# Kernel optimization log

Measured on AMD Instinct MI355X. Metric: run time of the kernel, lower is better.

## Reference

```python
import jax, jax.numpy as jnp
import numpy as np

NUM_HEADS = 16
HEAD_DIM = 64
D_DEC = 1024
D_ENC = 1024
R = 256  # kv_lora_rank
LN_EPS = 1e-5


def setup_inputs() -> dict:
    key = jax.random.key(0)
    ks = jax.random.split(key, 8)
    B, SQ, SK = 4, 2048, 4096
    query = jax.random.normal(ks[0], (B, SQ, D_DEC), dtype=jnp.float32)
    encoder_output = jax.random.normal(ks[1], (B, SK, D_ENC), dtype=jnp.float32)
    s = 0.02
    Wq = jax.random.normal(ks[2], (NUM_HEADS * HEAD_DIM, D_DEC), dtype=jnp.float32) * s
    Wkva = jax.random.normal(ks[3], (R, D_ENC), dtype=jnp.float32) * s
    ln_g = jnp.ones((R,), dtype=jnp.float32)
    ln_b = jnp.zeros((R,), dtype=jnp.float32)
    Wkvb = jax.random.normal(ks[4], (NUM_HEADS * 2 * HEAD_DIM, R), dtype=jnp.float32) * s
    Wout = jax.random.normal(ks[5], (D_DEC, NUM_HEADS * HEAD_DIM), dtype=jnp.float32) * s
    return {"query": query, "encoder_output": encoder_output, "Wq": Wq,
            "Wkva": Wkva, "ln_g": ln_g, "ln_b": ln_b, "Wkvb": Wkvb, "Wout": Wout}


def reference(query, encoder_output, Wq, Wkva, ln_g, ln_b, Wkvb, Wout):
    B, SQ, _ = query.shape
    SK = encoder_output.shape[1]
    H, Dh = NUM_HEADS, HEAD_DIM

    # q projection -> [B, H, SQ, Dh]
    q = jnp.einsum('bsd,ed->bse', query, Wq).reshape(B, SQ, H, Dh).transpose(0, 2, 1, 3)

    # low-rank KV compression + layernorm
    c = jnp.einsum('bsd,rd->bsr', encoder_output, Wkva)  # [B, SK, R]
    mu = jnp.mean(c, axis=-1, keepdims=True)
    var = jnp.mean(jnp.square(c - mu), axis=-1, keepdims=True)
    c = (c - mu) * jax.lax.rsqrt(var + LN_EPS) * ln_g + ln_b

    # decompress to K,V: [B, SK, H, 2*Dh] -> split
    kv = jnp.einsum('bsr,er->bse', c, Wkvb).reshape(B, SK, H, 2 * Dh).transpose(0, 2, 1, 3)
    k, v = kv[..., :Dh], kv[..., Dh:]

    scale = 1.0 / np.sqrt(Dh).astype(np.float32)
    scores = jnp.einsum('bhqd,bhkd->bhqk', q, k) * scale
    attn = jax.nn.softmax(scores, axis=-1)  # dropout is identity in eval / p=0
    o = jnp.einsum('bhqk,bhkd->bhqd', attn, v)
    o = o.transpose(0, 2, 1, 3).reshape(B, SQ, H * Dh)
    return jnp.einsum('bse,de->bsd', o, Wout)
```

## Files before the change

kernel.cpp:

```cpp
#include <hip/hip_runtime.h>

#define LOG2E 1.4426950408889634f

typedef __attribute__((ext_vector_type(8))) short short8;
typedef __attribute__((ext_vector_type(4))) float f32x4;

__device__ inline unsigned short f2bf(float f) {
  unsigned u = __float_as_uint(f);
  u += 0x7fffu + ((u >> 16) & 1u);
  return (unsigned short)(u >> 16);
}

#define MFMA16(a, b, c) __builtin_amdgcn_mfma_f32_16x16x32_bf16((a), (b), (c), 0, 0, 0)

#define GLDS16(gp, lp)                                                              \
  __builtin_amdgcn_global_load_lds((const __attribute__((address_space(1))) void*)(gp), \
                                   (__attribute__((address_space(3))) void*)(lp), 16, 0, 0)

__device__ inline f32x4 zero4() {
  f32x4 z = {0.f, 0.f, 0.f, 0.f};
  return z;
}

__global__ __launch_bounds__(256) void k_cast6(
    const float* __restrict__ e, const float* __restrict__ q, const float* __restrict__ wq,
    const float* __restrict__ wo, const float* __restrict__ wb, const float* __restrict__ wa,
    unsigned short* __restrict__ eo, unsigned short* __restrict__ qo, unsigned short* __restrict__ wqo,
    unsigned short* __restrict__ woo, unsigned short* __restrict__ wbo, unsigned short* __restrict__ wao) {
  int i = (blockIdx.x * 256 + threadIdx.x) * 4;
  const float* src;
  unsigned short* dst;
  int off;
  if (i < 16777216) { src = e; dst = eo; off = i; }
  else if (i < 25165824) { src = q; dst = qo; off = i - 16777216; }
  else if (i < 26214400) { src = wq; dst = wqo; off = i - 25165824; }
  else if (i < 27262976) { src = wo; dst = woo; off = i - 26214400; }
  else if (i < 27787264) { src = wb; dst = wbo; off = i - 27262976; }
  else { src = wa; dst = wao; off = i - 27787264; }
  float4 v = *(const float4*)(src + off);
  unsigned lo = (unsigned)f2bf(v.x) | ((unsigned)f2bf(v.y) << 16);
  unsigned hi = (unsigned)f2bf(v.z) | ((unsigned)f2bf(v.w) << 16);
  *(uint2*)(dst + off) = make_uint2(lo, hi);
}

__global__ __launch_bounds__(256, 2) void k_qproj(const unsigned short* __restrict__ A,
                                                  const unsigned short* __restrict__ Bw,
                                                  unsigned short* __restrict__ Qout) {
  __shared__ __align__(16) short As[128 * 32];
  __shared__ __align__(16) short Bs[128 * 32];
  const int K = 1024;
  int tid = threadIdx.x;
  int w = tid >> 6, lane = tid & 63, quad = lane >> 4, c = lane & 15;
  int m0 = blockIdx.x * 128, n0 = blockIdx.y * 128;
  int wm = (w >> 1) * 64, wn = (w & 1) * 64;
  f32x4 acc[4][4];
#pragma unroll
  for (int i = 0; i < 4; i++)
#pragma unroll
    for (int j = 0; j < 4; j++) acc[i][j] = zero4();

  for (int k0 = 0; k0 < K; k0 += 32) {
#pragma unroll
    for (int i = 0; i < 2; i++) {
      int seg = w * 2 + i;
      int bo = seg * 1024 + lane * 16;
      int row = bo >> 6, col = (bo & 63) >> 1;
      GLDS16(A + (size_t)(m0 + row) * K + k0 + col, (char*)As + seg * 1024);
      GLDS16(Bw + (size_t)(n0 + row) * K + k0 + col, (char*)Bs + seg * 1024);
    }
    __syncthreads();
    short8 af[4], bfr[4];
#pragma unroll
    for (int i = 0; i < 4; i++) {
      af[i] = *(const short8*)&As[(wm + i * 16 + c) * 32 + quad * 8];
      bfr[i] = *(const short8*)&Bs[(wn + i * 16 + c) * 32 + quad * 8];
    }
#pragma unroll
    for (int mi = 0; mi < 4; mi++)
#pragma unroll
      for (int ni = 0; ni < 4; ni++) acc[mi][ni] = MFMA16(af[mi], bfr[ni], acc[mi][ni]);
    __syncthreads();
  }
  const float scale = 0.125f * LOG2E;
#pragma unroll
  for (int mi = 0; mi < 4; mi++) {
    int rowb = m0 + wm + mi * 16 + quad * 4;
#pragma unroll
    for (int ni = 0; ni < 4; ni++) {
      int col = n0 + wn + ni * 16 + c;
      int h = col >> 6, d = col & 63;
#pragma unroll
      for (int r = 0; r < 4; r++) {
        int row = rowb + r;
        int b = row >> 11, sq = row & 2047;
        Qout[(((size_t)(b * 16 + h)) * 2048 + sq) * 64 + d] = f2bf(acc[mi][ni][r] * scale);
      }
    }
  }
}

__global__ __launch_bounds__(256, 2) void k_cln(const unsigned short* __restrict__ E,
                                                const unsigned short* __restrict__ Wa,
                                                const float* __restrict__ g, const float* __restrict__ bb,
                                                unsigned short* __restrict__ Cout) {
  __shared__ __align__(16) short As[64 * 32];
  __shared__ __align__(16) short Bs[256 * 32];
  __shared__ float redS[4][64], redQ[4][64];
  __shared__ float gS[256], bS[256];
  const int K = 1024;
  int tid = threadIdx.x;
  int w = tid >> 6, lane = tid & 63, quad = lane >> 4, c = lane & 15;
  int m0 = blockIdx.x * 64;
  gS[tid] = g[tid];
  bS[tid] = bb[tid];
  f32x4 acc[4][4];
#pragma unroll
  for (int i = 0; i < 4; i++)
#pragma unroll
    for (int j = 0; j < 4; j++) acc[i][j] = zero4();

  for (int k0 = 0; k0 < K; k0 += 32) {
    {
      int bo = w * 1024 + lane * 16;
      int row = bo >> 6, col = (bo & 63) >> 1;
      GLDS16(E + (size_t)(m0 + row) * K + k0 + col, (char*)As + w * 1024);
    }
#pragma unroll
    for (int i = 0; i < 4; i++) {
      int seg = w * 4 + i;
      int bo = seg * 1024 + lane * 16;
      int row = bo >> 6, col = (bo & 63) >> 1;
      GLDS16(Wa + (size_t)row * K + k0 + col, (char*)Bs + seg * 1024);
    }
    __syncthreads();
    short8 af[4], bfr[4];
#pragma unroll
    for (int i = 0; i < 4; i++) {
      af[i] = *(const short8*)&As[(i * 16 + c) * 32 + quad * 8];
      bfr[i] = *(const short8*)&Bs[(w * 64 + i * 16 + c) * 32 + quad * 8];
    }
#pragma unroll
    for (int mi = 0; mi < 4; mi++)
#pragma unroll
      for (int ni = 0; ni < 4; ni++) acc[mi][ni] = MFMA16(af[mi], bfr[ni], acc[mi][ni]);
    __syncthreads();
  }
  float ps[4][4], pq[4][4];
#pragma unroll
  for (int mi = 0; mi < 4; mi++)
#pragma unroll
    for (int r = 0; r < 4; r++) {
      float s = 0.f, q = 0.f;
#pragma unroll
      for (int ni = 0; ni < 4; ni++) {
        float x = acc[mi][ni][r];
        s += x;
        q += x * x;
      }
      for (int m = 1; m < 16; m <<= 1) {
        s += __shfl_xor(s, m, 64);
        q += __shfl_xor(q, m, 64);
      }
      ps[mi][r] = s;
      pq[mi][r] = q;
    }
  if (c == 0) {
#pragma unroll
    for (int mi = 0; mi < 4; mi++)
#pragma unroll
      for (int r = 0; r < 4; r++) {
        int row = mi * 16 + quad * 4 + r;
        redS[w][row] = ps[mi][r];
        redQ[w][row] = pq[mi][r];
      }
  }
  __syncthreads();
  float muv[4][4], rsv[4][4];
#pragma unroll
  for (int mi = 0; mi < 4; mi++)
#pragma unroll
    for (int r = 0; r < 4; r++) {
      int row = mi * 16 + quad * 4 + r;
      float S = redS[0][row] + redS[1][row] + redS[2][row] + redS[3][row];
      float Q = redQ[0][row] + redQ[1][row] + redQ[2][row] + redQ[3][row];
      float mu = S * (1.f / 256.f);
      float var = Q * (1.f / 256.f) - mu * mu;
      muv[mi][r] = mu;
      rsv[mi][r] = rsqrtf(var + 1e-5f);
    }
#pragma unroll
  for (int mi = 0; mi < 4; mi++)
#pragma unroll
    for (int ni = 0; ni < 4; ni++) {
      int col = w * 64 + ni * 16 + c;
#pragma unroll
      for (int r = 0; r < 4; r++) {
        int row = m0 + mi * 16 + quad * 4 + r;
        float y = (acc[mi][ni][r] - muv[mi][r]) * rsv[mi][r] * gS[col] + bS[col];
        Cout[(size_t)row * 256 + col] = f2bf(y);
      }
    }
}

__global__ __launch_bounds__(256, 2) void k_kv(const unsigned short* __restrict__ A,
                                               const unsigned short* __restrict__ Bw,
                                               unsigned short* __restrict__ Kb,
                                               unsigned short* __restrict__ Vb) {
  __shared__ __align__(16) short As[128 * 32];
  __shared__ __align__(16) short Bs[128 * 32];
  const int K = 256;
  int tid = threadIdx.x;
  int w = tid >> 6, lane = tid & 63, quad = lane >> 4, c = lane & 15;
  int m0 = blockIdx.x * 128, n0 = blockIdx.y * 128;
  int wm = (w >> 1) * 64, wn = (w & 1) * 64;
  f32x4 acc[4][4];
#pragma unroll
  for (int i = 0; i < 4; i++)
#pragma unroll
    for (int j = 0; j < 4; j++) acc[i][j] = zero4();

  for (int k0 = 0; k0 < K; k0 += 32) {
#pragma unroll
    for (int i = 0; i < 2; i++) {
      int seg = w * 2 + i;
      int bo = seg * 1024 + lane * 16;
      int row = bo >> 6, col = (bo & 63) >> 1;
      GLDS16(A + (size_t)(m0 + row) * K + k0 + col, (char*)As + seg * 1024);
      GLDS16(Bw + (size_t)(n0 + row) * K + k0 + col, (char*)Bs + seg * 1024);
    }
    __syncthreads();
    short8 af[4], bfr[4];
#pragma unroll
    for (int i = 0; i < 4; i++) {
      af[i] = *(const short8*)&As[(wm + i * 16 + c) * 32 + quad * 8];
      bfr[i] = *(const short8*)&Bs[(wn + i * 16 + c) * 32 + quad * 8];
    }
#pragma unroll
    for (int mi = 0; mi < 4; mi++)
#pragma unroll
      for (int ni = 0; ni < 4; ni++) acc[mi][ni] = MFMA16(af[mi], bfr[ni], acc[mi][ni]);
    __syncthreads();
  }
#pragma unroll
  for (int mi = 0; mi < 4; mi++) {
    int rowb = m0 + wm + mi * 16 + quad * 4;
#pragma unroll
    for (int ni = 0; ni < 4; ni++) {
      int col = n0 + wn + ni * 16 + c;
      int h = col >> 7, rr = col & 127;
#pragma unroll
      for (int r = 0; r < 4; r++) {
        int row = rowb + r;
        int b = row >> 12, sk = row & 4095;
        float x = acc[mi][ni][r];
        if (rr < 64)
          Kb[(((size_t)(b * 16 + h)) * 4096 + sk) * 64 + rr] = f2bf(x);
        else
          Vb[(((size_t)(b * 16 + h)) * 64 + (rr - 64)) * 4096 + sk] = f2bf(x);
      }
    }
  }
}

__global__ __launch_bounds__(256, 4) void k_attn(const unsigned short* __restrict__ Qb,
                                                 const unsigned short* __restrict__ Kb,
                                                 const unsigned short* __restrict__ Vb,
                                                 unsigned short* __restrict__ Ob) {
  __shared__ __align__(16) short KVs[2 * 64 * 64];
  __shared__ __align__(16) short Ps[4][2048];
  int tid = threadIdx.x;
  int w = tid >> 6, lane = tid & 63, quad = lane >> 4, c = lane & 15;
  int r8 = lane >> 3, pc = lane & 7;
  int qt = blockIdx.x, bh = blockIdx.y;

  const char* Kg = (const char*)Kb + (size_t)bh * 524288;
  const char* Vg = (const char*)Vb + (size_t)bh * 524288;
  const unsigned short* Qv = Qb + ((size_t)bh * 2048 + qt * 128 + w * 32) * 64 + c * 64 + quad * 8;

  const char* sg[4];
  int step = (w < 2) ? 8192 : 128;
#pragma unroll
  for (int i = 0; i < 4; i++) {
    int seg = w * 4 + i;
    if (w < 2) {
      int row = seg * 8 + r8;
      sg[i] = Kg + row * 128 + ((pc ^ r8) << 4);
    } else {
      int vrow = (seg - 8) * 8 + r8;
      sg[i] = Vg + (size_t)vrow * 8192 + ((pc ^ r8) << 4);
    }
  }

  int c7 = c & 7;
  int kb0 = c * 128 + ((quad ^ c7) << 4);
  int kb1 = c * 128 + (((quad + 4) ^ c7) << 4);
  const char* KsB0 = (const char*)KVs + kb0;
  const char* KsB1 = (const char*)KVs + kb1;
  const char* VsB0 = (const char*)KVs + 8192 + kb0;
  const char* VsB1 = (const char*)KVs + 8192 + kb1;
  char* pwm[4];
#pragma unroll
  for (int mt = 0; mt < 4; mt++)
    pwm[mt] = (char*)Ps[w] + c * 128 + (quad & 1) * 8 + ((((mt * 2) ^ (quad >> 1) ^ c7)) << 4);
  const char* pr0 = (const char*)Ps[w] + c * 128 + ((quad ^ c7) << 4);
  const char* pr1 = (const char*)Ps[w] + c * 128 + (((quad + 4) ^ c7) << 4);

  short8 qf[2][2];
#pragma unroll
  for (int nt = 0; nt < 2; nt++)
#pragma unroll
    for (int h = 0; h < 2; h++) qf[nt][h] = *(const short8*)(Qv + nt * 1024 + h * 32);

  f32x4 O[2][4];
  float lp[2] = {0.f, 0.f};
#pragma unroll
  for (int i = 0; i < 2; i++)
#pragma unroll
    for (int j = 0; j < 4; j++) O[i][j] = zero4();

#pragma unroll
  for (int i = 0; i < 4; i++) {
    GLDS16(sg[i], (char*)KVs + (w * 4 + i) * 1024);
    sg[i] += step;
  }

  for (int kt = 0; kt < 64; kt++) {
    __syncthreads();
#pragma unroll
    for (int mt = 0; mt < 4; mt++) {
      short8 kf0 = *(const short8*)(KsB0 + mt * 2048);
      short8 kf1 = *(const short8*)(KsB1 + mt * 2048);
      f32x4 s0 = MFMA16(kf0, qf[0][0], zero4());
      s0 = MFMA16(kf1, qf[0][1], s0);
      f32x4 s1 = MFMA16(kf0, qf[1][0], zero4());
      s1 = MFMA16(kf1, qf[1][1], s1);
#pragma unroll
      for (int nt = 0; nt < 2; nt++) {
        f32x4 s = nt ? s1 : s0;
        float p0 = __builtin_amdgcn_exp2f(s[0]);
        float p1 = __builtin_amdgcn_exp2f(s[1]);
        float p2 = __builtin_amdgcn_exp2f(s[2]);
        float p3 = __builtin_amdgcn_exp2f(s[3]);
        lp[nt] += (p0 + p1) + (p2 + p3);
        unsigned r0 = __float_as_uint(p0) + 0x8000u;
        unsigned r1 = __float_as_uint(p1) + 0x8000u;
        unsigned r2 = __float_as_uint(p2) + 0x8000u;
        unsigned r3 = __float_as_uint(p3) + 0x8000u;
        unsigned lo = __builtin_amdgcn_perm(r1, r0, 0x07060302u);
        unsigned hi = __builtin_amdgcn_perm(r3, r2, 0x07060302u);
        *(uint2*)(pwm[mt] + nt * 2048) = make_uint2(lo, hi);
      }
    }
#pragma unroll
    for (int kk = 0; kk < 2; kk++) {
      const char* VsB = kk ? VsB1 : VsB0;
      const char* pr = kk ? pr1 : pr0;
      short8 vf[4];
#pragma unroll
      for (int dt = 0; dt < 4; dt++) vf[dt] = *(const short8*)(VsB + dt * 2048);
#pragma unroll
      for (int mo = 0; mo < 2; mo++) {
        short8 pf = *(const short8*)(pr + mo * 2048);
#pragma unroll
        for (int dt = 0; dt < 4; dt++) O[mo][dt] = MFMA16(pf, vf[dt], O[mo][dt]);
      }
    }
    __syncthreads();
    if (kt < 63) {
#pragma unroll
      for (int i = 0; i < 4; i++) {
        GLDS16(sg[i], (char*)KVs + (w * 4 + i) * 1024);
        sg[i] += step;
      }
    }
  }

#pragma unroll
  for (int nt = 0; nt < 2; nt++) {
    lp[nt] += __shfl_xor(lp[nt], 16, 64);
    lp[nt] += __shfl_xor(lp[nt], 32, 64);
  }
  int b = bh >> 4, h = bh & 15;
#pragma unroll
  for (int mo = 0; mo < 2; mo++) {
#pragma unroll
    for (int r = 0; r < 4; r++) {
      float inv = __builtin_amdgcn_rcpf(__shfl(lp[mo], quad * 4 + r, 64));
      int sq = qt * 128 + w * 32 + mo * 16 + quad * 4 + r;
#pragma unroll
      for (int dt = 0; dt < 4; dt++)
        Ob[((size_t)b * 2048 + sq) * 1024 + h * 64 + dt * 16 + c] = f2bf(O[mo][dt][r] * inv);
    }
  }
}

__global__ __launch_bounds__(256, 2) void k_out(const unsigned short* __restrict__ A,
                                                const unsigned short* __restrict__ Bw,
                                                float* __restrict__ Out) {
  __shared__ __align__(16) short As[128 * 32];
  __shared__ __align__(16) short Bs[128 * 32];
  const int K = 1024;
  int tid = threadIdx.x;
  int w = tid >> 6, lane = tid & 63, quad = lane >> 4, c = lane & 15;
  int m0 = blockIdx.x * 128, n0 = blockIdx.y * 128;
  int wm = (w >> 1) * 64, wn = (w & 1) * 64;
  f32x4 acc[4][4];
#pragma unroll
  for (int i = 0; i < 4; i++)
#pragma unroll
    for (int j = 0; j < 4; j++) acc[i][j] = zero4();

  for (int k0 = 0; k0 < K; k0 += 32) {
#pragma unroll
    for (int i = 0; i < 2; i++) {
      int seg = w * 2 + i;
      int bo = seg * 1024 + lane * 16;
      int row = bo >> 6, col = (bo & 63) >> 1;
      GLDS16(A + (size_t)(m0 + row) * K + k0 + col, (char*)As + seg * 1024);
      GLDS16(Bw + (size_t)(n0 + row) * K + k0 + col, (char*)Bs + seg * 1024);
    }
    __syncthreads();
    short8 af[4], bfr[4];
#pragma unroll
    for (int i = 0; i < 4; i++) {
      af[i] = *(const short8*)&As[(wm + i * 16 + c) * 32 + quad * 8];
      bfr[i] = *(const short8*)&Bs[(wn + i * 16 + c) * 32 + quad * 8];
    }
#pragma unroll
    for (int mi = 0; mi < 4; mi++)
#pragma unroll
      for (int ni = 0; ni < 4; ni++) acc[mi][ni] = MFMA16(af[mi], bfr[ni], acc[mi][ni]);
    __syncthreads();
  }
#pragma unroll
  for (int mi = 0; mi < 4; mi++) {
    int rowb = m0 + wm + mi * 16 + quad * 4;
#pragma unroll
    for (int ni = 0; ni < 4; ni++) {
      int col = n0 + wn + ni * 16 + c;
#pragma unroll
      for (int r = 0; r < 4; r++) Out[(size_t)(rowb + r) * 1024 + col] = acc[mi][ni][r];
    }
  }
}

extern "C" void kernel_launch(void* const* d_in, const int* in_sizes, int n_in,
                              void* d_out, int out_size, void* d_ws, size_t ws_size,
                              hipStream_t stream) {
  const float* query = (const float*)d_in[0];
  const float* enc = (const float*)d_in[1];
  const float* Wq = (const float*)d_in[2];
  const float* Wkva = (const float*)d_in[3];
  const float* ln_g = (const float*)d_in[4];
  const float* ln_b = (const float*)d_in[5];
  const float* Wkvb = (const float*)d_in[6];
  const float* Wout = (const float*)d_in[7];
  if (ws_size < 81264640) return;

  char* ws = (char*)d_ws;
  unsigned short* wq_bf = (unsigned short*)(ws + 0);
  unsigned short* wa_bf = (unsigned short*)(ws + 2097152);
  unsigned short* wb_bf = (unsigned short*)(ws + 2621440);
  unsigned short* wo_bf = (unsigned short*)(ws + 3670016);
  unsigned short* qproj = (unsigned short*)(ws + 5767168);
  unsigned short* cln = (unsigned short*)(ws + 22544384);
  unsigned short* ebf_v = (unsigned short*)(ws + 30932992);
  unsigned short* qin_o = (unsigned short*)(ws + 64487424);
  unsigned short* kbuf = (unsigned short*)d_out;

  k_cast6<<<27392, 256, 0, stream>>>(enc, query, Wq, Wout, Wkvb, Wkva,
                                     ebf_v, qin_o, wq_bf, wo_bf, wb_bf, wa_bf);

  k_qproj<<<dim3(64, 8), 256, 0, stream>>>(qin_o, wq_bf, qproj);
  k_cln<<<256, 256, 0, stream>>>(ebf_v, wa_bf, ln_g, ln_b, cln);
  k_kv<<<dim3(128, 16), 256, 0, stream>>>(cln, wb_bf, kbuf, ebf_v);
  k_attn<<<dim3(16, 64), 256, 0, stream>>>(qproj, kbuf, ebf_v, qin_o);
  k_out<<<dim3(64, 8), 256, 0, stream>>>(qin_o, wo_bf, (float*)d_out);
}
```

Measured before the change: 448.1 us.

## Rewrite attention kernel with 32x32 MFMA, register-resident P and fragment-ordered K/V

The attention kernel moves from 16x16x32 to 32x32x16 bf16 MFMA with 128-thread blocks. Each wave now owns 64 query rows. P is converted with v_cvt_pk_bf16 and rearranged between lanes with permlane32_swap, so it stays in registers instead of passing through an LDS scratch buffer. k_kv now writes K and V already laid out in MFMA fragment order per 64-key tile, which lets them be streamed into a double-buffered LDS with plain linear loads and waited on with explicit vmcnt barriers. This removes LDS round trips and swizzle arithmetic, at the cost of higher register pressure and fewer waves per block.

```diff
diff --git a/kernel.cpp b/kernel.cpp
--- a/kernel.cpp
+++ b/kernel.cpp
@@ -4,6 +4,8 @@
 
 typedef __attribute__((ext_vector_type(8))) short short8;
 typedef __attribute__((ext_vector_type(4))) float f32x4;
+typedef __attribute__((ext_vector_type(16))) float f32x16;
+typedef __attribute__((ext_vector_type(4))) unsigned u32x4;
 
 __device__ inline unsigned short f2bf(float f) {
   unsigned u = __float_as_uint(f);
@@ -12,6 +14,7 @@
 }
 
 #define MFMA16(a, b, c) __builtin_amdgcn_mfma_f32_16x16x32_bf16((a), (b), (c), 0, 0, 0)
+#define MFMA32(a, b, c) __builtin_amdgcn_mfma_f32_32x32x16_bf16((a), (b), (c), 0, 0, 0)
 
 #define GLDS16(gp, lp)                                                              \
   __builtin_amdgcn_global_load_lds((const __attribute__((address_space(1))) void*)(gp), \
@@ -20,6 +23,18 @@
 __device__ inline f32x4 zero4() {
   f32x4 z = {0.f, 0.f, 0.f, 0.f};
   return z;
+}
+__device__ inline f32x16 zero16() {
+  f32x16 z = {0.f, 0.f, 0.f, 0.f, 0.f, 0.f, 0.f, 0.f, 0.f, 0.f, 0.f, 0.f, 0.f, 0.f, 0.f, 0.f};
+  return z;
+}
+__device__ inline unsigned cvtpk_bf16(float a, float b) {
+  unsigned r;
+  asm("v_cvt_pk_bf16_f32 %0, %1, %2" : "=v"(r) : "v"(a), "v"(b));
+  return r;
+}
+__device__ inline void plswap(unsigned& a, unsigned& b) {
+  asm("v_permlane32_swap_b32 %0, %1" : "+v"(a), "+v"(b));
 }
 
 __global__ __launch_bounds__(256) void k_cast6(
@@ -252,144 +267,126 @@
       for (int r = 0; r < 4; r++) {
         int row = rowb + r;
         int b = row >> 12, sk = row & 4095;
+        int kt = sk >> 6, ki = sk & 63;
+        size_t base = ((size_t)(b * 16 + h)) * 262144 + (size_t)kt * 4096;
         float x = acc[mi][ni][r];
-        if (rr < 64)
-          Kb[(((size_t)(b * 16 + h)) * 4096 + sk) * 64 + rr] = f2bf(x);
-        else
-          Vb[(((size_t)(b * 16 + h)) * 64 + (rr - 64)) * 4096 + sk] = f2bf(x);
-      }
-    }
-  }
-}
-
-__global__ __launch_bounds__(256, 4) void k_attn(const unsigned short* __restrict__ Qb,
+        if (rr < 64) {
+          int d = rr;
+          int half = ki >> 5, l31k = ki & 31, ds = d >> 4, dhi = (d >> 3) & 1, j = d & 7;
+          Kb[base + (size_t)((half * 4 + ds) * 64 + l31k + 32 * dhi) * 8 + j] = f2bf(x);
+        } else {
+          int d = rr - 64;
+          int dt = d >> 5, sg = ki >> 4, khi = (ki >> 3) & 1, j = ki & 7;
+          Vb[base + (size_t)((dt * 4 + sg) * 64 + (d & 31) + 32 * khi) * 8 + j] = f2bf(x);
+        }
+      }
+    }
+  }
+}
+
+__global__ __launch_bounds__(128, 2) void k_attn(const unsigned short* __restrict__ Qb,
                                                  const unsigned short* __restrict__ Kb,
                                                  const unsigned short* __restrict__ Vb,
                                                  unsigned short* __restrict__ Ob) {
-  __shared__ __align__(16) short KVs[2 * 64 * 64];
-  __shared__ __align__(16) short Ps[4][2048];
+  __shared__ __align__(16) short KVs[16384];
   int tid = threadIdx.x;
-  int w = tid >> 6, lane = tid & 63, quad = lane >> 4, c = lane & 15;
-  int r8 = lane >> 3, pc = lane & 7;
+  int w = tid >> 6, lane = tid & 63;
+  int l31 = lane & 31, hi = lane >> 5;
   int qt = blockIdx.x, bh = blockIdx.y;
 
   const char* Kg = (const char*)Kb + (size_t)bh * 524288;
   const char* Vg = (const char*)Vb + (size_t)bh * 524288;
-  const unsigned short* Qv = Qb + ((size_t)bh * 2048 + qt * 128 + w * 32) * 64 + c * 64 + quad * 8;
-
-  const char* sg[4];
-  int step = (w < 2) ? 8192 : 128;
-#pragma unroll
-  for (int i = 0; i < 4; i++) {
-    int seg = w * 4 + i;
-    if (w < 2) {
-      int row = seg * 8 + r8;
-      sg[i] = Kg + row * 128 + ((pc ^ r8) << 4);
-    } else {
-      int vrow = (seg - 8) * 8 + r8;
-      sg[i] = Vg + (size_t)vrow * 8192 + ((pc ^ r8) << 4);
-    }
-  }
-
-  int c7 = c & 7;
-  int kb0 = c * 128 + ((quad ^ c7) << 4);
-  int kb1 = c * 128 + (((quad + 4) ^ c7) << 4);
-  const char* KsB0 = (const char*)KVs + kb0;
-  const char* KsB1 = (const char*)KVs + kb1;
-  const char* VsB0 = (const char*)KVs + 8192 + kb0;
-  const char* VsB1 = (const char*)KVs + 8192 + kb1;
-  char* pwm[4];
-#pragma unroll
-  for (int mt = 0; mt < 4; mt++)
-    pwm[mt] = (char*)Ps[w] + c * 128 + (quad & 1) * 8 + ((((mt * 2) ^ (quad >> 1) ^ c7)) << 4);
-  const char* pr0 = (const char*)Ps[w] + c * 128 + ((quad ^ c7) << 4);
-  const char* pr1 = (const char*)Ps[w] + c * 128 + (((quad + 4) ^ c7) << 4);
-
-  short8 qf[2][2];
-#pragma unroll
-  for (int nt = 0; nt < 2; nt++)
-#pragma unroll
-    for (int h = 0; h < 2; h++) qf[nt][h] = *(const short8*)(Qv + nt * 1024 + h * 32);
-
-  f32x4 O[2][4];
+  const char* sgbase = (w ? Vg : Kg) + lane * 16;
+
+  const unsigned short* Qrow = Qb + ((size_t)bh * 2048 + qt * 128 + w * 64 + l31) * 64 + hi * 8;
+  short8 qf[2][4];
+#pragma unroll
+  for (int qb = 0; qb < 2; qb++)
+#pragma unroll
+    for (int ds = 0; ds < 4; ds++) qf[qb][ds] = *(const short8*)(Qrow + qb * 2048 + ds * 16);
+
+  f32x16 O[2][2];
   float lp[2] = {0.f, 0.f};
 #pragma unroll
   for (int i = 0; i < 2; i++)
 #pragma unroll
-    for (int j = 0; j < 4; j++) O[i][j] = zero4();
-
-#pragma unroll
-  for (int i = 0; i < 4; i++) {
-    GLDS16(sg[i], (char*)KVs + (w * 4 + i) * 1024);
-    sg[i] += step;
-  }
+    for (int j = 0; j < 2; j++) O[i][j] = zero16();
+
+#pragma unroll
+  for (int i = 0; i < 8; i++) GLDS16(sgbase + i * 1024, (char*)KVs + w * 8192 + i * 1024);
+#pragma unroll
+  for (int i = 0; i < 8; i++) GLDS16(sgbase + 8192 + i * 1024, (char*)KVs + 16384 + w * 8192 + i * 1024);
+  sgbase += 16384;
 
   for (int kt = 0; kt < 64; kt++) {
-    __syncthreads();
-#pragma unroll
-    for (int mt = 0; mt < 4; mt++) {
-      short8 kf0 = *(const short8*)(KsB0 + mt * 2048);
-      short8 kf1 = *(const short8*)(KsB1 + mt * 2048);
-      f32x4 s0 = MFMA16(kf0, qf[0][0], zero4());
-      s0 = MFMA16(kf1, qf[0][1], s0);
-      f32x4 s1 = MFMA16(kf0, qf[1][0], zero4());
-      s1 = MFMA16(kf1, qf[1][1], s1);
-#pragma unroll
-      for (int nt = 0; nt < 2; nt++) {
-        f32x4 s = nt ? s1 : s0;
-        float p0 = __builtin_amdgcn_exp2f(s[0]);
-        float p1 = __builtin_amdgcn_exp2f(s[1]);
-        float p2 = __builtin_amdgcn_exp2f(s[2]);
-        float p3 = __builtin_amdgcn_exp2f(s[3]);
-        lp[nt] += (p0 + p1) + (p2 + p3);
-        unsigned r0 = __float_as_uint(p0) + 0x8000u;
-        unsigned r1 = __float_as_uint(p1) + 0x8000u;
-        unsigned r2 = __float_as_uint(p2) + 0x8000u;
-        unsigned r3 = __float_as_uint(p3) + 0x8000u;
-        unsigned lo = __builtin_amdgcn_perm(r1, r0, 0x07060302u);
-        unsigned hi = __builtin_amdgcn_perm(r3, r2, 0x07060302u);
-        *(uint2*)(pwm[mt] + nt * 2048) = make_uint2(lo, hi);
-      }
-    }
-#pragma unroll
-    for (int kk = 0; kk < 2; kk++) {
-      const char* VsB = kk ? VsB1 : VsB0;
-      const char* pr = kk ? pr1 : pr0;
-      short8 vf[4];
-#pragma unroll
-      for (int dt = 0; dt < 4; dt++) vf[dt] = *(const short8*)(VsB + dt * 2048);
-#pragma unroll
-      for (int mo = 0; mo < 2; mo++) {
-        short8 pf = *(const short8*)(pr + mo * 2048);
-#pragma unroll
-        for (int dt = 0; dt < 4; dt++) O[mo][dt] = MFMA16(pf, vf[dt], O[mo][dt]);
-      }
-    }
-    __syncthreads();
-    if (kt < 63) {
-#pragma unroll
-      for (int i = 0; i < 4; i++) {
-        GLDS16(sg[i], (char*)KVs + (w * 4 + i) * 1024);
-        sg[i] += step;
-      }
-    }
-  }
-
-#pragma unroll
-  for (int nt = 0; nt < 2; nt++) {
-    lp[nt] += __shfl_xor(lp[nt], 16, 64);
-    lp[nt] += __shfl_xor(lp[nt], 32, 64);
-  }
-  int b = bh >> 4, h = bh & 15;
-#pragma unroll
-  for (int mo = 0; mo < 2; mo++) {
-#pragma unroll
-    for (int r = 0; r < 4; r++) {
-      float inv = __builtin_amdgcn_rcpf(__shfl(lp[mo], quad * 4 + r, 64));
-      int sq = qt * 128 + w * 32 + mo * 16 + quad * 4 + r;
-#pragma unroll
-      for (int dt = 0; dt < 4; dt++)
-        Ob[((size_t)b * 2048 + sq) * 1024 + h * 64 + dt * 16 + c] = f2bf(O[mo][dt][r] * inv);
+    if (kt == 63)
+      asm volatile("s_waitcnt vmcnt(0)\n\ts_barrier" ::: "memory");
+    else
+      asm volatile("s_waitcnt vmcnt(8)\n\ts_barrier" ::: "memory");
+
+    const char* Kl = (const char*)KVs + (kt & 1) * 16384 + lane * 16;
+    const char* Vl = Kl + 8192;
+
+#pragma unroll
+    for (int h = 0; h < 2; h++) {
+      short8 kf[4];
+#pragma unroll
+      for (int ds = 0; ds < 4; ds++) kf[ds] = *(const short8*)(Kl + (h * 4 + ds) * 1024);
+      short8 paf[2][2];
+#pragma unroll
+      for (int qb = 0; qb < 2; qb++) {
+        f32x16 S = zero16();
+#pragma unroll
+        for (int ds = 0; ds < 4; ds++) S = MFMA32(kf[ds], qf[qb][ds], S);
+        float pp[8];
+        unsigned u[8];
+#pragma unroll
+        for (int m = 0; m < 8; m++) {
+          float p0 = __builtin_amdgcn_exp2f(S[2 * m]);
+          float p1 = __builtin_amdgcn_exp2f(S[2 * m + 1]);
+          pp[m] = p0 + p1;
+          u[m] = cvtpk_bf16(p0, p1);
+        }
+        lp[qb] += ((pp[0] + pp[1]) + (pp[2] + pp[3])) + ((pp[4] + pp[5]) + (pp[6] + pp[7]));
+        plswap(u[0], u[2]);
+        plswap(u[1], u[3]);
+        plswap(u[4], u[6]);
+        plswap(u[5], u[7]);
+        u32x4 w0 = {u[0], u[1], u[2], u[3]};
+        u32x4 w1 = {u[4], u[5], u[6], u[7]};
+        paf[qb][0] = __builtin_bit_cast(short8, w0);
+        paf[qb][1] = __builtin_bit_cast(short8, w1);
+      }
+#pragma unroll
+      for (int dt = 0; dt < 2; dt++)
+#pragma unroll
+        for (int s2 = 0; s2 < 2; s2++) {
+          short8 vf = *(const short8*)(Vl + (dt * 4 + h * 2 + s2) * 1024);
+#pragma unroll
+          for (int qb = 0; qb < 2; qb++) O[qb][dt] = MFMA32(paf[qb][s2], vf, O[qb][dt]);
+        }
+    }
+    asm volatile("s_barrier" ::: "memory");
+    if (kt < 62) {
+#pragma unroll
+      for (int i = 0; i < 8; i++)
+        GLDS16(sgbase + i * 1024, (char*)KVs + (kt & 1) * 16384 + w * 8192 + i * 1024);
+      sgbase += 8192;
+    }
+  }
+
+#pragma unroll
+  for (int qb = 0; qb < 2; qb++) lp[qb] += __shfl_xor(lp[qb], 32, 64);
+  int b = bh >> 4, hh = bh & 15;
+#pragma unroll
+  for (int qb = 0; qb < 2; qb++) {
+#pragma unroll
+    for (int r = 0; r < 16; r++) {
+      int qrow = (r & 3) + 8 * (r >> 2) + 4 * hi;
+      float inv = __builtin_amdgcn_rcpf(__shfl(lp[qb], qrow, 64));
+      size_t orow = ((size_t)b * 2048 + qt * 128 + w * 64 + qb * 32 + qrow) * 1024 + hh * 64 + l31;
+      Ob[orow] = f2bf(O[qb][0][r] * inv);
+      Ob[orow + 32] = f2bf(O[qb][1][r] * inv);
     }
   }
 }
@@ -474,6 +471,6 @@
   k_qproj<<<dim3(64, 8), 256, 0, stream>>>(qin_o, wq_bf, qproj);
   k_cln<<<256, 256, 0, stream>>>(ebf_v, wa_bf, ln_g, ln_b, cln);
   k_kv<<<dim3(128, 16), 256, 0, stream>>>(cln, wb_bf, kbuf, ebf_v);
-  k_attn<<<dim3(16, 64), 256, 0, stream>>>(qproj, kbuf, ebf_v, qin_o);
+  k_attn<<<dim3(16, 64), 128, 0, stream>>>(qproj, kbuf, ebf_v, qin_o);
   k_out<<<dim3(64, 8), 256, 0, stream>>>(qin_o, wo_bf, (float*)d_out);
 }
```

After: 403.8 us. 1.11x faster.
